# Kernel optimization log

Hardware: AMD Instinct MI355X
Metric: run time of the kernel (lower is better)

## Reference

```python
import jax, jax.numpy as jnp
import numpy as np

B, M, K = 32, 64, 36
DS, DX, DQ, H = 512, 128, 512, 256


def setup_inputs() -> dict:
    key = jax.random.key(0)
    ks = jax.random.split(key, 11)
    sc = lambda fan_in: 1.0 / np.sqrt(fan_in)
    return {
        "s2": jax.random.normal(ks[0], (B, M, DS), jnp.float32),
        "x0": jax.random.normal(ks[1], (B, K, DX), jnp.float32),
        "q": jax.random.normal(ks[2], (B, DQ), jnp.float32),
        # score MLP: Linear(DS+DX+DQ -> H), ReLU, Linear(H -> 1)
        "score_w1": jax.random.normal(ks[3], (DS + DX + DQ, H), jnp.float32) * sc(DS + DX + DQ),
        "score_b1": jax.random.normal(ks[4], (H,), jnp.float32) * 0.01,
        "score_w2": jax.random.normal(ks[5], (H, 1), jnp.float32) * sc(H),
        "score_b2": jax.random.normal(ks[6], (1,), jnp.float32) * 0.01,
        # h MLP: Linear(DS -> H), ReLU, Linear(H -> DX)
        "h_w1": jax.random.normal(ks[7], (DS, H), jnp.float32) * sc(DS),
        "h_b1": jax.random.normal(ks[8], (H,), jnp.float32) * 0.01,
        "h_w2": jax.random.normal(ks[9], (H, DX), jnp.float32) * sc(H),
        "h_b2": jax.random.normal(ks[10], (DX,), jnp.float32) * 0.01,
    }


def reference(s2, x0, q, score_w1, score_b1, score_w2, score_b2, h_w1, h_b1, h_w2, h_b2):
    ds = s2.shape[-1]
    dx = x0.shape[-1]
    # First score Linear over concat [s_exp, x_exp, q_exp] decomposes into
    # block matmuls (same math as Linear on the concat, no 4D concat tensor).
    w_s = score_w1[:ds]            # (DS, H)
    w_x = score_w1[ds:ds + dx]     # (DX, H)
    w_q = score_w1[ds + dx:]       # (DQ, H)
    pre_s = jnp.einsum('bmd,dh->bmh', s2, w_s)   # (b, m, H)
    pre_x = jnp.einsum('bkd,dh->bkh', x0, w_x)   # (b, k, H)
    pre_q = q @ w_q                              # (b, H)
    hidden = jax.nn.relu(pre_s[:, :, None, :] + pre_x[:, None, :, :]
                         + pre_q[:, None, None, :] + score_b1)  # (b, m, k, H)
    logits = jnp.einsum('bmkh,h->bmk', hidden, score_w2[:, 0]) + score_b2[0]
    att = jax.nn.softmax(logits, axis=1)         # softmax over m
    h_s = jax.nn.relu(s2 @ h_w1 + h_b1) @ h_w2 + h_b2  # (b, m, DX)
    agg = jnp.einsum('bmk,bmf->bkf', att, h_s)   # (b, k, DX)
    return jnp.concatenate([x0, agg], axis=-1)   # (b, k, 2*DX)
```

## Files before the change

### kernel.cpp

```cpp
#include <hip/hip_runtime.h>

#define B_  32
#define M_  64
#define K_  36
#define DS_ 512
#define DX_ 128
#define DQ_ 512
#define H_  256

#define S2B 1024
#define PXB 288
#define QPB 32

__global__ __launch_bounds__(512, 6) void kern1(
    const float* __restrict__ s2,
    const float* __restrict__ x0,
    const float* __restrict__ q,
    const float* __restrict__ score_w1,
    const float* __restrict__ score_b1,
    const float* __restrict__ h_w1,
    const float* __restrict__ h_b1,
    const float* __restrict__ h_w2,
    float* __restrict__ pre_s,
    float* __restrict__ px,
    float* __restrict__ qpre,
    float* __restrict__ hs)
{
    __shared__ float As[4 * DS_];
    __shared__ float comb[4 * H_];
    __shared__ float hre[4 * H_];

    const int t   = threadIdx.x;
    const int bid = blockIdx.x;
    const int h   = t & 255;
    const int kh  = __builtin_amdgcn_readfirstlane(t >> 8);

    if (bid < S2B) {
        const int tile = bid >> 1, mat = bid & 1;
        const float* W = mat ? h_w1 : score_w1;

        {
            const float* Asrc = s2 + (size_t)tile * 4 * DS_;
            *(float4*)&As[t * 4] = *(const float4*)(Asrc + t * 4);
        }
        __syncthreads();

        const float* Wp = W + (size_t)(kh * 256) * H_ + h;
        const int ab = kh * 256;

        float acc[4];
        #pragma unroll
        for (int r = 0; r < 4; ++r) acc[r] = 0.f;

        #pragma unroll 2
        for (int k = 0; k < 256; k += 4) {
            const float b0 = Wp[(size_t)(k + 0) * H_];
            const float b1 = Wp[(size_t)(k + 1) * H_];
            const float b2 = Wp[(size_t)(k + 2) * H_];
            const float b3 = Wp[(size_t)(k + 3) * H_];
            #pragma unroll
            for (int r = 0; r < 4; ++r) {
                const float4 a = *(const float4*)&As[r * DS_ + ab + k];
                acc[r] = fmaf(a.x, b0, acc[r]);
                acc[r] = fmaf(a.y, b1, acc[r]);
                acc[r] = fmaf(a.z, b2, acc[r]);
                acc[r] = fmaf(a.w, b3, acc[r]);
            }
        }

        if (kh) {
            #pragma unroll
            for (int r = 0; r < 4; ++r) comb[r * H_ + h] = acc[r];
        }
        __syncthreads();

        if (!mat) {
            if (!kh) {
                float* dst = pre_s + (size_t)tile * 4 * H_ + h;
                #pragma unroll
                for (int r = 0; r < 4; ++r)
                    dst[(size_t)r * H_] = acc[r] + comb[r * H_ + h];
            }
        } else {
            if (!kh) {
                const float b1v = h_b1[h];
                #pragma unroll
                for (int r = 0; r < 4; ++r)
                    hre[r * H_ + h] =
                        fmaxf(acc[r] + comb[r * H_ + h] + b1v, 0.f);
            }
            __syncthreads();

            const int row = t >> 7;
            const int f   = t & 127;
            const float* w2p = h_w2 + f;
            float o0 = 0.f, o1 = 0.f, o2 = 0.f, o3 = 0.f;
            #pragma unroll 2
            for (int k = 0; k < H_; k += 4) {
                o0 = fmaf(hre[row * H_ + k + 0], w2p[(size_t)(k + 0) * DX_], o0);
                o1 = fmaf(hre[row * H_ + k + 1], w2p[(size_t)(k + 1) * DX_], o1);
                o2 = fmaf(hre[row * H_ + k + 2], w2p[(size_t)(k + 2) * DX_], o2);
                o3 = fmaf(hre[row * H_ + k + 3], w2p[(size_t)(k + 3) * DX_], o3);
            }
            hs[((size_t)tile * 4 + row) * DX_ + f] = (o0 + o1) + (o2 + o3);
        }

    } else if (bid < S2B + PXB) {
        const int tile = bid - S2B;

        if (t < 128) {
            const float* Asrc = x0 + (size_t)tile * 4 * DX_;
            *(float4*)&As[t * 4] = *(const float4*)(Asrc + t * 4);
        }
        __syncthreads();

        const float* Wp = score_w1 + (size_t)(DS_ + kh * 64) * H_ + h;
        const int ab = kh * 64;

        float acc[4];
        #pragma unroll
        for (int r = 0; r < 4; ++r) acc[r] = 0.f;

        #pragma unroll 2
        for (int k = 0; k < 64; k += 4) {
            const float b0 = Wp[(size_t)(k + 0) * H_];
            const float b1 = Wp[(size_t)(k + 1) * H_];
            const float b2 = Wp[(size_t)(k + 2) * H_];
            const float b3 = Wp[(size_t)(k + 3) * H_];
            #pragma unroll
            for (int r = 0; r < 4; ++r) {
                const float4 a = *(const float4*)&As[r * DX_ + ab + k];
                acc[r] = fmaf(a.x, b0, acc[r]);
                acc[r] = fmaf(a.y, b1, acc[r]);
                acc[r] = fmaf(a.z, b2, acc[r]);
                acc[r] = fmaf(a.w, b3, acc[r]);
            }
        }
        if (kh) {
            #pragma unroll
            for (int r = 0; r < 4; ++r) comb[r * H_ + h] = acc[r];
        }
        __syncthreads();
        if (!kh) {
            const float b1v = score_b1[h];
            float* dst = px + (size_t)tile * 4 * H_ + h;
            #pragma unroll
            for (int r = 0; r < 4; ++r)
                dst[(size_t)r * H_] = acc[r] + comb[r * H_ + h] + b1v;
        }

    } else {
        const int b = bid - (S2B + PXB);

        if (t < 128) {
            const float* Asrc = q + (size_t)b * DQ_;
            *(float4*)&As[t * 4] = *(const float4*)(Asrc + t * 4);
        }
        __syncthreads();

        const float* wq = score_w1 + (size_t)(DS_ + DX_ + kh * 256) * H_ + h;
        const int qb = kh * 256;
        float a0 = 0.f, a1 = 0.f, a2 = 0.f, a3 = 0.f;
        #pragma unroll 2
        for (int d = 0; d < 256; d += 4) {
            const float4 q4 = *(const float4*)&As[qb + d];
            a0 = fmaf(q4.x, wq[(size_t)(d + 0) * H_], a0);
            a1 = fmaf(q4.y, wq[(size_t)(d + 1) * H_], a1);
            a2 = fmaf(q4.z, wq[(size_t)(d + 2) * H_], a2);
            a3 = fmaf(q4.w, wq[(size_t)(d + 3) * H_], a3);
        }
        const float s = (a0 + a1) + (a2 + a3);
        if (kh) comb[h] = s;
        __syncthreads();
        if (!kh) qpre[(size_t)b * H_ + h] = s + comb[h];
    }
}

__global__ __launch_bounds__(256) void kern3(
    const float* __restrict__ pre_s,
    const float* __restrict__ px,
    const float* __restrict__ qpre,
    const float* __restrict__ score_w2,
    const float* __restrict__ hs,
    const float* __restrict__ h_b2,
    const float* __restrict__ x0,
    float* __restrict__ out)
{
    __shared__ float logit[M_];
    __shared__ float att[M_];
    __shared__ float pr[DX_];

    const int t    = threadIdx.x;
    const int bk   = blockIdx.x;
    const int b    = bk / K_;
    const int lane = t & 63, wave = t >> 6;
    const int hq   = lane << 2;

    float4 c4, v4;
    {
        const float4 qv = *(const float4*)(qpre + (size_t)b * H_ + hq);
        const float4 pv = *(const float4*)(px + (size_t)bk * H_ + hq);
        c4.x = qv.x + pv.x; c4.y = qv.y + pv.y;
        c4.z = qv.z + pv.z; c4.w = qv.w + pv.w;
        v4 = *(const float4*)(score_w2 + hq);
    }

    const float* ps = pre_s + (size_t)b * M_ * H_;
    #pragma unroll 2
    for (int mi = 0; mi < 16; ++mi) {
        const int m = wave * 16 + mi;
        const float4 p = *(const float4*)(ps + (size_t)m * H_ + hq);
        float x = fmaxf(p.x + c4.x, 0.f) * v4.x
                + fmaxf(p.y + c4.y, 0.f) * v4.y
                + fmaxf(p.z + c4.z, 0.f) * v4.z
                + fmaxf(p.w + c4.w, 0.f) * v4.w;
        #pragma unroll
        for (int off = 32; off > 0; off >>= 1)
            x += __shfl_xor(x, off, 64);
        if (lane == 0) logit[m] = x;
    }
    __syncthreads();

    if (wave == 0) {
        const float L = logit[lane];
        float mx = L;
        #pragma unroll
        for (int off = 32; off > 0; off >>= 1)
            mx = fmaxf(mx, __shfl_xor(mx, off, 64));
        const float e = expf(L - mx);
        float sm = e;
        #pragma unroll
        for (int off = 32; off > 0; off >>= 1)
            sm += __shfl_xor(sm, off, 64);
        att[lane] = e / sm;
    }
    __syncthreads();

    const int f = t & 127, mh = t >> 7;
    {
        const float* hsp = hs + ((size_t)b * M_ + mh * 32) * DX_ + f;
        float r = 0.f;
        #pragma unroll 4
        for (int m2 = 0; m2 < 32; ++m2)
            r = fmaf(att[mh * 32 + m2], hsp[(size_t)m2 * DX_], r);
        if (mh) pr[f] = r;
        __syncthreads();
        if (!mh)
            out[(size_t)bk * (2 * DX_) + DX_ + f] = r + pr[f] + h_b2[f];
    }
    if (t < DX_)
        out[(size_t)bk * (2 * DX_) + t] = x0[(size_t)bk * DX_ + t];
}

extern "C" void kernel_launch(void* const* d_in, const int* in_sizes, int n_in,
                              void* d_out, int out_size, void* d_ws, size_t ws_size,
                              hipStream_t stream) {
    (void)in_sizes; (void)n_in; (void)out_size; (void)ws_size;
    const float* s2       = (const float*)d_in[0];
    const float* x0       = (const float*)d_in[1];
    const float* q        = (const float*)d_in[2];
    const float* score_w1 = (const float*)d_in[3];
    const float* score_b1 = (const float*)d_in[4];
    const float* score_w2 = (const float*)d_in[5];
    const float* h_w1     = (const float*)d_in[7];
    const float* h_b1     = (const float*)d_in[8];
    const float* h_w2     = (const float*)d_in[9];
    const float* h_b2     = (const float*)d_in[10];
    float* out = (float*)d_out;

    float* ws    = (float*)d_ws;
    float* pre_s = ws;
    float* px    = pre_s + (size_t)B_ * M_ * H_;
    float* qpre  = px    + (size_t)B_ * K_ * H_;
    float* hs    = qpre  + (size_t)B_ * H_;

    kern1<<<S2B + PXB + QPB, 512, 0, stream>>>(
        s2, x0, q, score_w1, score_b1, h_w1, h_b1, h_w2,
        pre_s, px, qpre, hs);
    kern3<<<B_ * K_, 256, 0, stream>>>(pre_s, px, qpre, score_w2, hs, h_b2,
                                       x0, out);
}
```

Baseline: 131.1 us.

## Use 8-row s2 tiles with 2x4 register blocking in first-layer GEMM

```diff
diff --git a/kernel.cpp b/kernel.cpp
--- a/kernel.cpp
+++ b/kernel.cpp
@@ -8,11 +8,11 @@
 #define DQ_ 512
 #define H_  256
 
-#define S2B 1024
+#define S2B 512
 #define PXB 288
 #define QPB 32
 
-__global__ __launch_bounds__(512, 6) void kern1(
+__global__ __launch_bounds__(512, 4) void kern1(
     const float* __restrict__ s2,
     const float* __restrict__ x0,
     const float* __restrict__ q,
@@ -26,87 +26,132 @@
     float* __restrict__ qpre,
     float* __restrict__ hs)
 {
-    __shared__ float As[4 * DS_];
-    __shared__ float comb[4 * H_];
-    __shared__ float hre[4 * H_];
+    __shared__ float As[8 * DS_];
+    __shared__ float comb[8 * H_];
+    __shared__ float hre[8 * H_];
 
     const int t   = threadIdx.x;
     const int bid = blockIdx.x;
-    const int h   = t & 255;
+    const int l   = t & 63;
     const int kh  = __builtin_amdgcn_readfirstlane(t >> 8);
 
     if (bid < S2B) {
         const int tile = bid >> 1, mat = bid & 1;
+        const int rg   = __builtin_amdgcn_readfirstlane((t >> 6) & 3);
         const float* W = mat ? h_w1 : score_w1;
 
         {
-            const float* Asrc = s2 + (size_t)tile * 4 * DS_;
-            *(float4*)&As[t * 4] = *(const float4*)(Asrc + t * 4);
-        }
-        __syncthreads();
-
-        const float* Wp = W + (size_t)(kh * 256) * H_ + h;
+            const float* Asrc = s2 + (size_t)tile * 8 * DS_;
+            *(float4*)&As[t * 4]        = *(const float4*)(Asrc + t * 4);
+            *(float4*)&As[t * 4 + 2048] = *(const float4*)(Asrc + t * 4 + 2048);
+        }
+        __syncthreads();
+
+        const float4* Wq = (const float4*)(W + (size_t)(kh * 256) * H_) + l;
+        const int r0 = rg * 2;
         const int ab = kh * 256;
 
-        float acc[4];
-        #pragma unroll
-        for (int r = 0; r < 4; ++r) acc[r] = 0.f;
+        float4 acc0 = make_float4(0.f, 0.f, 0.f, 0.f);
+        float4 acc1 = make_float4(0.f, 0.f, 0.f, 0.f);
 
         #pragma unroll 2
         for (int k = 0; k < 256; k += 4) {
-            const float b0 = Wp[(size_t)(k + 0) * H_];
-            const float b1 = Wp[(size_t)(k + 1) * H_];
-            const float b2 = Wp[(size_t)(k + 2) * H_];
-            const float b3 = Wp[(size_t)(k + 3) * H_];
-            #pragma unroll
-            for (int r = 0; r < 4; ++r) {
-                const float4 a = *(const float4*)&As[r * DS_ + ab + k];
-                acc[r] = fmaf(a.x, b0, acc[r]);
-                acc[r] = fmaf(a.y, b1, acc[r]);
-                acc[r] = fmaf(a.z, b2, acc[r]);
-                acc[r] = fmaf(a.w, b3, acc[r]);
+            const float4 w0  = Wq[(size_t)(k + 0) * 64];
+            const float4 w1  = Wq[(size_t)(k + 1) * 64];
+            const float4 w2v = Wq[(size_t)(k + 2) * 64];
+            const float4 w3  = Wq[(size_t)(k + 3) * 64];
+            const float4 a0 = *(const float4*)&As[(r0 + 0) * DS_ + ab + k];
+            const float4 a1 = *(const float4*)&As[(r0 + 1) * DS_ + ab + k];
+            acc0.x = fmaf(a0.x, w0.x, acc0.x);
+            acc0.y = fmaf(a0.x, w0.y, acc0.y);
+            acc0.z = fmaf(a0.x, w0.z, acc0.z);
+            acc0.w = fmaf(a0.x, w0.w, acc0.w);
+            acc0.x = fmaf(a0.y, w1.x, acc0.x);
+            acc0.y = fmaf(a0.y, w1.y, acc0.y);
+            acc0.z = fmaf(a0.y, w1.z, acc0.z);
+            acc0.w = fmaf(a0.y, w1.w, acc0.w);
+            acc0.x = fmaf(a0.z, w2v.x, acc0.x);
+            acc0.y = fmaf(a0.z, w2v.y, acc0.y);
+            acc0.z = fmaf(a0.z, w2v.z, acc0.z);
+            acc0.w = fmaf(a0.z, w2v.w, acc0.w);
+            acc0.x = fmaf(a0.w, w3.x, acc0.x);
+            acc0.y = fmaf(a0.w, w3.y, acc0.y);
+            acc0.z = fmaf(a0.w, w3.z, acc0.z);
+            acc0.w = fmaf(a0.w, w3.w, acc0.w);
+            acc1.x = fmaf(a1.x, w0.x, acc1.x);
+            acc1.y = fmaf(a1.x, w0.y, acc1.y);
+            acc1.z = fmaf(a1.x, w0.z, acc1.z);
+            acc1.w = fmaf(a1.x, w0.w, acc1.w);
+            acc1.x = fmaf(a1.y, w1.x, acc1.x);
+            acc1.y = fmaf(a1.y, w1.y, acc1.y);
+            acc1.z = fmaf(a1.y, w1.z, acc1.z);
+            acc1.w = fmaf(a1.y, w1.w, acc1.w);
+            acc1.x = fmaf(a1.z, w2v.x, acc1.x);
+            acc1.y = fmaf(a1.z, w2v.y, acc1.y);
+            acc1.z = fmaf(a1.z, w2v.z, acc1.z);
+            acc1.w = fmaf(a1.z, w2v.w, acc1.w);
+            acc1.x = fmaf(a1.w, w3.x, acc1.x);
+            acc1.y = fmaf(a1.w, w3.y, acc1.y);
+            acc1.z = fmaf(a1.w, w3.z, acc1.z);
+            acc1.w = fmaf(a1.w, w3.w, acc1.w);
+        }
+
+        if (kh) {
+            *(float4*)&comb[(r0 + 0) * H_ + l * 4] = acc0;
+            *(float4*)&comb[(r0 + 1) * H_ + l * 4] = acc1;
+        }
+        __syncthreads();
+        if (!kh) {
+            const float4 c0 = *(const float4*)&comb[(r0 + 0) * H_ + l * 4];
+            const float4 c1 = *(const float4*)&comb[(r0 + 1) * H_ + l * 4];
+            if (!mat) {
+                float4 o0 = make_float4(acc0.x + c0.x, acc0.y + c0.y,
+                                        acc0.z + c0.z, acc0.w + c0.w);
+                float4 o1 = make_float4(acc1.x + c1.x, acc1.y + c1.y,
+                                        acc1.z + c1.z, acc1.w + c1.w);
+                float* dst = pre_s + ((size_t)tile * 8 + r0) * H_ + l * 4;
+                *(float4*)dst        = o0;
+                *(float4*)(dst + H_) = o1;
+            } else {
+                const float4 bv = *(const float4*)(h_b1 + l * 4);
+                float4 o0, o1;
+                o0.x = fmaxf(acc0.x + c0.x + bv.x, 0.f);
+                o0.y = fmaxf(acc0.y + c0.y + bv.y, 0.f);
+                o0.z = fmaxf(acc0.z + c0.z + bv.z, 0.f);
+                o0.w = fmaxf(acc0.w + c0.w + bv.w, 0.f);
+                o1.x = fmaxf(acc1.x + c1.x + bv.x, 0.f);
+                o1.y = fmaxf(acc1.y + c1.y + bv.y, 0.f);
+                o1.z = fmaxf(acc1.z + c1.z + bv.z, 0.f);
+                o1.w = fmaxf(acc1.w + c1.w + bv.w, 0.f);
+                *(float4*)&hre[(r0 + 0) * H_ + l * 4] = o0;
+                *(float4*)&hre[(r0 + 1) * H_ + l * 4] = o1;
             }
         }
-
-        if (kh) {
-            #pragma unroll
-            for (int r = 0; r < 4; ++r) comb[r * H_ + h] = acc[r];
-        }
-        __syncthreads();
-
-        if (!mat) {
-            if (!kh) {
-                float* dst = pre_s + (size_t)tile * 4 * H_ + h;
-                #pragma unroll
-                for (int r = 0; r < 4; ++r)
-                    dst[(size_t)r * H_] = acc[r] + comb[r * H_ + h];
-            }
-        } else {
-            if (!kh) {
-                const float b1v = h_b1[h];
-                #pragma unroll
-                for (int r = 0; r < 4; ++r)
-                    hre[r * H_ + h] =
-                        fmaxf(acc[r] + comb[r * H_ + h] + b1v, 0.f);
-            }
+        if (mat) {
             __syncthreads();
-
-            const int row = t >> 7;
-            const int f   = t & 127;
-            const float* w2p = h_w2 + f;
-            float o0 = 0.f, o1 = 0.f, o2 = 0.f, o3 = 0.f;
+            const int row = __builtin_amdgcn_readfirstlane(t >> 6);
+            const int f0  = l * 2;
+            const float* w2p = h_w2 + f0;
+            float s0 = 0.f, s1 = 0.f;
             #pragma unroll 2
             for (int k = 0; k < H_; k += 4) {
-                o0 = fmaf(hre[row * H_ + k + 0], w2p[(size_t)(k + 0) * DX_], o0);
-                o1 = fmaf(hre[row * H_ + k + 1], w2p[(size_t)(k + 1) * DX_], o1);
-                o2 = fmaf(hre[row * H_ + k + 2], w2p[(size_t)(k + 2) * DX_], o2);
-                o3 = fmaf(hre[row * H_ + k + 3], w2p[(size_t)(k + 3) * DX_], o3);
+                const float4 hv = *(const float4*)&hre[row * H_ + k];
+                const float2 wa = *(const float2*)(w2p + (size_t)(k + 0) * DX_);
+                const float2 wb = *(const float2*)(w2p + (size_t)(k + 1) * DX_);
+                const float2 wc = *(const float2*)(w2p + (size_t)(k + 2) * DX_);
+                const float2 wd = *(const float2*)(w2p + (size_t)(k + 3) * DX_);
+                s0 = fmaf(hv.x, wa.x, s0); s1 = fmaf(hv.x, wa.y, s1);
+                s0 = fmaf(hv.y, wb.x, s0); s1 = fmaf(hv.y, wb.y, s1);
+                s0 = fmaf(hv.z, wc.x, s0); s1 = fmaf(hv.z, wc.y, s1);
+                s0 = fmaf(hv.w, wd.x, s0); s1 = fmaf(hv.w, wd.y, s1);
             }
-            hs[((size_t)tile * 4 + row) * DX_ + f] = (o0 + o1) + (o2 + o3);
+            *(float2*)(hs + ((size_t)tile * 8 + row) * DX_ + f0) =
+                make_float2(s0, s1);
         }
 
     } else if (bid < S2B + PXB) {
         const int tile = bid - S2B;
+        const int h    = t & 255;
 
         if (t < 128) {
             const float* Asrc = x0 + (size_t)tile * 4 * DX_;
@@ -151,6 +196,7 @@
 
     } else {
         const int b = bid - (S2B + PXB);
+        const int h = t & 255;
 
         if (t < 128) {
             const float* Asrc = q + (size_t)b * DQ_;
```

Result: slower. 153.0 us (+16.7%).
